# Optimization experiments

Hardware: AMD Instinct MI355X
Metric: run time of the kernel (lower is better)

The kernel has to match this reference:

```python
import jax, jax.numpy as jnp
import numpy as np
import math

B, S, D, H = 4, 2048, 2048, 16
HD = D // H  # 128


def _alibi_slopes(n_heads):
    # standard ALiBi slopes: 2^(-8/n * (h+1))
    return jnp.asarray([2.0 ** (-8.0 / n_heads * (h + 1)) for h in range(n_heads)], dtype=jnp.float32)


def setup_inputs() -> dict:
    key = jax.random.key(0)
    ks = jax.random.split(key, 10)
    w = lambda k: jax.random.normal(k, (D, D), dtype=jnp.float32) * 0.02
    b = lambda k: jax.random.normal(k, (D,), dtype=jnp.float32) * 0.01
    return {
        "hidden_states": jax.random.normal(ks[0], (B, S, D), dtype=jnp.float32),
        "Wq": w(ks[1]), "bq": b(ks[2]),
        "Wk": w(ks[3]), "bk": b(ks[4]),
        "Wv": w(ks[5]), "bv": b(ks[6]),
        "Wo": w(ks[7]), "bo": b(ks[8]),
        "alibi_slopes": _alibi_slopes(H),
    }


def reference(hidden_states, Wq, bq, Wk, bk, Wv, bv, Wo, bo, alibi_slopes):
    Bn, t, _ = hidden_states.shape
    split = lambda x: x.reshape(Bn, t, H, HD).transpose(0, 2, 1, 3)  # [B,H,S,hd]
    q = split(hidden_states @ Wq.T + bq)
    k = split(hidden_states @ Wk.T + bk)
    v = split(hidden_states @ Wv.T + bv)

    scores = jnp.einsum("bhsd,bhtd->bhst", q, k)  # [B,H,S,S]
    pos = jnp.arange(t)
    # alibi bias added BEFORE the 1/sqrt(hd) scaling, as in the torch code
    rel = (pos[None, :] - pos[:, None]).astype(scores.dtype)  # j - i
    bias = alibi_slopes[:, None, None] * rel  # [H,S,S]
    scores = (scores + bias[None]) / math.sqrt(HD)
    # grok-style tanh rescaling
    scores = 30.0 * jnp.tanh(scores / 30.0)
    causal = pos[:, None] >= pos[None, :]  # [S,S]
    scores = jnp.where(causal[None, None], scores, -jnp.inf)
    probs = jax.nn.softmax(scores, axis=-1)
    ctx = jnp.einsum("bhst,bhtd->bhsd", probs, v)
    ctx = ctx.transpose(0, 2, 1, 3).reshape(Bn, t, D)
    return ctx @ Wo.T + bo
```

## Files before the change

### kernel.cpp

```cpp
#include <hip/hip_runtime.h>

typedef unsigned int u32;
typedef unsigned short u16;
typedef __bf16 bf16x8 __attribute__((ext_vector_type(8)));
typedef float f32x4 __attribute__((ext_vector_type(4)));


__device__ __forceinline__ u16 f2bf(float f) {
  u32 u = __builtin_bit_cast(u32, f);
  u32 r = u + 0x7fffu + ((u >> 16) & 1u);
  return (u16)(r >> 16);
}

__device__ __forceinline__ void gload_lds16(const void* g, void* l) {
  __builtin_amdgcn_global_load_lds(
      (__attribute__((address_space(1))) void*)(g),
      (__attribute__((address_space(3))) void*)(l), 16, 0, 0);
}


__global__ __launch_bounds__(256) void convert_kernel(
    const float* __restrict__ hs, const float* __restrict__ wq,
    const float* __restrict__ wk, const float* __restrict__ wv,
    const float* __restrict__ wo,
    u16* __restrict__ hsb, u16* __restrict__ wqb, u16* __restrict__ wkb,
    u16* __restrict__ wvb, u16* __restrict__ wob) {
  long t = (long)blockIdx.x * 256 + threadIdx.x;
  const float* src;
  u16* dst;
  long off;
  if (t < 2097152) {
    src = hs; dst = hsb; off = t << 3;
  } else {
    long u = t - 2097152;
    int wi = (int)(u >> 19);
    off = (u & 524287) << 3;
    if (wi == 0)      { src = wq; dst = wqb; }
    else if (wi == 1) { src = wk; dst = wkb; }
    else if (wi == 2) { src = wv; dst = wvb; }
    else              { src = wo; dst = wob; }
  }
  float4 a = *(const float4*)(src + off);
  float4 b = *(const float4*)(src + off + 4);
  uint4 o;
  o.x = (u32)f2bf(a.x) | ((u32)f2bf(a.y) << 16);
  o.y = (u32)f2bf(a.z) | ((u32)f2bf(a.w) << 16);
  o.z = (u32)f2bf(b.x) | ((u32)f2bf(b.y) << 16);
  o.w = (u32)f2bf(b.z) | ((u32)f2bf(b.w) << 16);
  *(uint4*)(dst + off) = o;
}


template <int OF32>
__global__ __launch_bounds__(512, 2) void gemm256_kernel(
    const u16* __restrict__ A, const u16* __restrict__ Bw,
    const float* __restrict__ bias0, const float* __restrict__ bias1,
    const float* __restrict__ bias2, void* __restrict__ o0,
    void* __restrict__ o1, void* __restrict__ o2, int m_tiles, int n_tiles) {
  __shared__ __align__(16) char L[2][2][2][16384];

  const int tid = threadIdx.x;
  const int lane = tid & 63, w = tid >> 6;
  const int lr = lane & 15, lk = lane >> 4;
  const int wm = (w >> 2) * 128, wn = (w & 3) * 64;

  const int bid = blockIdx.x;
  const int xcd = bid & 7, loc = bid >> 3;
  const int npx = n_tiles >> 3;
  const int n_idx = xcd * npx + loc % npx;
  const int m_idx = loc / npx;
  const int m0 = m_idx * 256, n0 = n_idx * 256;

  const char* Ab = (const char*)A;
  const char* Bb = (const char*)Bw;
  const char* gA[2];
  const char* gB[2];
#pragma unroll
  for (int j = 0; j < 2; j++) {
    const int o = j * 8192 + tid * 16;
    const int row = o >> 6;
    const int c = (o & 63) ^ (((row >> 1) & 3) << 4);
    gA[j] = Ab + (size_t)(m0 + row) * 4096 + c;
    gB[j] = Bb + (size_t)(n0 + row) * 4096 + c;
  }

  auto stage = [&](int t, int kh, int isB) {
    char* Ld = &L[t & 1][isB][kh][0] + tid * 16;
    const int gof = t * 128 + kh * 64;
#pragma unroll
    for (int j = 0; j < 2; j++)
      gload_lds16((isB ? gB[j] : gA[j]) + gof, Ld + j * 8192);
  };
  auto rdA = [&](bf16x8* dst, int buf, int kh, int mset) {
#pragma unroll
    for (int m = 0; m < 4; m++) {
      const int row = wm + mset * 64 + m * 16 + lr;
      const int c = (lk * 16) ^ (((row >> 1) & 3) << 4);
      dst[m] = *(const bf16x8*)(&L[buf][0][kh][0] + row * 64 + c);
    }
  };
  auto rdB = [&](bf16x8* dst, int buf, int kh) {
#pragma unroll
    for (int n = 0; n < 4; n++) {
      const int row = wn + n * 16 + lr;
      const int c = (lk * 16) ^ (((row >> 1) & 3) << 4);
      dst[n] = *(const bf16x8*)(&L[buf][1][kh][0] + row * 64 + c);
    }
  };

  f32x4 acc[2][4][4];
#pragma unroll
  for (int s = 0; s < 2; s++)
#pragma unroll
    for (int m = 0; m < 4; m++)
#pragma unroll
      for (int n = 0; n < 4; n++) acc[s][m][n] = {0.f, 0.f, 0.f, 0.f};

  auto mm = [&](f32x4 (&ac)[4][4], bf16x8* a_, bf16x8* b_) {
    __builtin_amdgcn_s_setprio(1);
#pragma unroll
    for (int m = 0; m < 4; m++)
#pragma unroll
      for (int n = 0; n < 4; n++)
        ac[m][n] = __builtin_amdgcn_mfma_f32_16x16x32_bf16(a_[m], b_[n],
                                                           ac[m][n], 0, 0, 0);
    __builtin_amdgcn_s_setprio(0);
  };

  stage(0, 0, 0); stage(0, 0, 1); stage(0, 1, 0); stage(0, 1, 1);

  bf16x8 aP[4], aQ[4], b0[4], b1[4];
  for (int t = 0; t < 32; ++t) {
    const int buf = t & 1;
    const int t1 = (t + 1 < 32) ? t + 1 : 31;
    asm volatile("s_waitcnt vmcnt(4)" ::: "memory");
    asm volatile("s_barrier" ::: "memory");
    rdA(aP, buf, 0, 0);
    rdB(b0, buf, 0);
    stage(t1, 0, 0);
    if (t) mm(acc[1], aQ, b1);
    rdA(aQ, buf, 0, 1);
    stage(t1, 0, 1);
    mm(acc[0], aP, b0);
    asm volatile("s_waitcnt vmcnt(4)" ::: "memory");
    asm volatile("s_barrier" ::: "memory");
    rdA(aP, buf, 1, 0);
    rdB(b1, buf, 1);
    stage(t1, 1, 0);
    mm(acc[1], aQ, b0);
    rdA(aQ, buf, 1, 1);
    stage(t1, 1, 1);
    mm(acc[0], aP, b1);
  }
  mm(acc[1], aQ, b1);

  const float* bias;
  void* op;
  int nl0;
  if (OF32) {
    bias = bias0; op = o0; nl0 = n0;
  } else {
    const int seg = n0 >> 11;
    bias = seg == 0 ? bias0 : (seg == 1 ? bias1 : bias2);
    op = seg == 0 ? o0 : (seg == 1 ? o1 : o2);
    nl0 = n0 & 2047;
  }
#pragma unroll
  for (int n = 0; n < 4; n++) {
    const int col = nl0 + wn + n * 16 + lr;
    const float bv = bias[col];
#pragma unroll
    for (int s = 0; s < 2; s++)
#pragma unroll
      for (int m = 0; m < 4; m++) {
        const int grow = m0 + wm + s * 64 + m * 16 + lk * 4;
#pragma unroll
        for (int r = 0; r < 4; r++) {
          const float v = acc[s][m][n][r] + bv;
          if (OF32)
            ((float*)op)[(size_t)(grow + r) * 2048 + col] = v;
          else
            ((u16*)op)[(size_t)(grow + r) * 2048 + col] = f2bf(v);
        }
      }
  }
}


__global__ __launch_bounds__(512, 2) void attn_kernel(
    const u16* __restrict__ Qm, const u16* __restrict__ Km,
    const u16* __restrict__ Vm, const float* __restrict__ slopes,
    u16* __restrict__ ctx) {
  __shared__ __align__(16) char Ks[2][64 * 256];
  __shared__ __align__(16) char Vt[128 * 128];
  __shared__ __align__(16) char Pb[8][16 * 128];

  const int bid = blockIdx.x;
  const int sw = (bid & 7) * 64 + (bid >> 3);
  const int bh = sw >> 3, pi = sw & 7;
  const int b = bh >> 4, h = bh & 15;
  const int NTA = 2 * pi + 2;

  const int tid = threadIdx.x;
  const int lane = tid & 63, w = tid >> 6;
  const int lr = lane & 15, lk = lane >> 4;

  const char* Qb = (const char*)Qm + (size_t)b * 2048 * 4096 + h * 256;
  const char* Kb = (const char*)Km + (size_t)b * 2048 * 4096 + h * 256;
  const char* Vb = (const char*)Vm + (size_t)b * 2048 * 4096 + h * 256;

  const float SCALE = 0.08838834764831845f;
  const float sl_c = slopes[h] * SCALE;

  const float C1 = 1.4426950408889634f;
  const float C3 = -5.343315e-4f;
  const float C5 = 2.374806e-7f;
  const float C7 = -1.068005e-10f;

  float zo[16];
#pragma unroll
  for (int nb = 0; nb < 4; nb++)
#pragma unroll
    for (int r = 0; r < 4; r++)
      zo[nb * 4 + r] = sl_c * (float)((lr - lk * 4) + nb * 16 - r);

  const int vd0 = (tid & 15) * 8;
  const int vkv2 = tid >> 4;

  uint4 vr0, vr1;

  auto kvt_of = [&](int it) { return it < NTA ? it : it - NTA; };

  auto stageK = [&](int it, int buf) {
    const int kv0 = kvt_of(it) * 64;
#pragma unroll
    for (int j = 0; j < 2; j++) {
      const int o = j * 8192 + tid * 16;
      const int row = o >> 8, c = (o & 255) ^ ((row & 7) << 4);
      gload_lds16(Kb + (size_t)(kv0 + row) * 4096 + c, Ks[buf] + o);
    }
  };
  auto loadV = [&](int it) {
    const int kv0 = kvt_of(it) * 64;
    vr0 = *(const uint4*)(Vb + (size_t)(kv0 + vkv2 * 2) * 4096 + vd0 * 2);
    vr1 = *(const uint4*)(Vb + (size_t)(kv0 + vkv2 * 2 + 1) * 4096 + vd0 * 2);
  };
  auto writeV = [&]() {
    const u32* p0 = (const u32*)&vr0;
    const u32* p1 = (const u32*)&vr1;
#pragma unroll
    for (int wd = 0; wd < 4; wd++) {
      const u32 ev = __builtin_amdgcn_perm(p1[wd], p0[wd], 0x05040100u);
      const u32 od = __builtin_amdgcn_perm(p1[wd], p0[wd], 0x07060302u);
      const int d0_ = vd0 + 2 * wd, d1_ = d0_ + 1;
      *(u32*)(Vt + d0_ * 128 +
              ((vkv2 * 4) ^ (((d0_ ^ (d0_ >> 3)) & 7) << 4))) = ev;
      *(u32*)(Vt + d1_ * 128 +
              ((vkv2 * 4) ^ (((d1_ ^ (d1_ >> 3)) & 7) << 4))) = od;
    }
  };

  bf16x8 qf[4];
  f32x4 pv[8];
  float rs[4];
  int q0 = 0;

  stageK(0, 0);
  loadV(0);

  for (int it = 0; it < 34; ++it) {
    const int kb = it & 1;
    const int kv0 = kvt_of(it) * 64;

    if (it == 0 || it == NTA) {
      const int st = (it == 0) ? pi : (15 - pi);
      q0 = st * 128 + w * 16;
#pragma unroll
      for (int kc = 0; kc < 4; kc++)
        qf[kc] =
            *(const bf16x8*)(Qb + (size_t)(q0 + lr) * 4096 + kc * 64 + lk * 16);
#pragma unroll
      for (int i = 0; i < 8; i++) pv[i] = {0.f, 0.f, 0.f, 0.f};
      rs[0] = rs[1] = rs[2] = rs[3] = 0.f;
    }

    __syncthreads();
    writeV();
    asm volatile("s_waitcnt vmcnt(0)" ::: "memory");
    __syncthreads();

    if (it + 1 < 34) {
      stageK(it + 1, kb ^ 1);
      loadV(it + 1);
    }

    f32x4 sc[4];
    __builtin_amdgcn_s_setprio(1);
#pragma unroll
    for (int nb = 0; nb < 4; nb++) {
      f32x4 a = {0.f, 0.f, 0.f, 0.f};
      const int krow = nb * 16 + lr;
#pragma unroll
      for (int kc = 0; kc < 4; kc++) {
        const int off = krow * 256 + ((kc * 64 + lk * 16) ^ ((krow & 7) << 4));
        bf16x8 kf = *(const bf16x8*)(Ks[kb] + off);
        a = __builtin_amdgcn_mfma_f32_16x16x32_bf16(qf[kc], kf, a, 0, 0, 0);
      }
      sc[nb] = a;
    }
    __builtin_amdgcn_s_setprio(0);

    const bool diag = (it < NTA) ? (it >= NTA - 2) : (it >= 32);
    const float sb = sl_c * (float)(kv0 - q0);
#pragma unroll
    for (int nb = 0; nb < 4; nb++) {
#pragma unroll
      for (int r = 0; r < 4; r++) {
        float z = fmaf(sc[nb][r], SCALE, zo[nb * 4 + r] + sb);
        z = __builtin_amdgcn_fmed3f(z, -16.0f, 16.0f);
        const float u2 = z * z;
        float hh = fmaf(u2, C7, C5);
        hh = fmaf(u2, hh, C3);
        hh = fmaf(u2, hh, C1);
        float p = exp2f(z * hh);
        if (diag) {
          const int kv = kv0 + nb * 16 + lr;
          const int q = q0 + lk * 4 + r;
          p = (kv <= q) ? p : 0.0f;
        }
        rs[r] += p;
        const int qq = lk * 4 + r;
        const int off = qq * 128 + (((nb * 16 + lr) * 2) ^ ((qq & 7) << 4));
        const u32 ub = __builtin_bit_cast(u32, p);
        *(u16*)(Pb[w] + off) = (u16)((ub + 0x8000u) >> 16);
      }
    }

    __builtin_amdgcn_s_setprio(1);
#pragma unroll
    for (int kc = 0; kc < 2; kc++) {
      const int poff = lr * 128 + ((kc * 64 + lk * 16) ^ ((lr & 7) << 4));
      bf16x8 pf = *(const bf16x8*)(Pb[w] + poff);
#pragma unroll
      for (int db = 0; db < 8; db++) {
        const int d = db * 16 + lr;
        const int voff =
            d * 128 + ((kc * 64 + lk * 16) ^ (((d ^ (d >> 3)) & 7) << 4));
        bf16x8 vf = *(const bf16x8*)(Vt + voff);
        pv[db] = __builtin_amdgcn_mfma_f32_16x16x32_bf16(pf, vf, pv[db], 0, 0, 0);
      }
    }
    __builtin_amdgcn_s_setprio(0);

    if (it == NTA - 1 || it == 33) {
      float inv[4];
#pragma unroll
      for (int r = 0; r < 4; r++) {
        float s = rs[r];
        s += __shfl_xor(s, 1);
        s += __shfl_xor(s, 2);
        s += __shfl_xor(s, 4);
        s += __shfl_xor(s, 8);
        inv[r] = 1.0f / s;
      }
      const size_t baserow = (size_t)b * 2048 + q0 + lk * 4;
#pragma unroll
      for (int db = 0; db < 8; db++)
#pragma unroll
        for (int r = 0; r < 4; r++)
          ctx[(baserow + r) * 2048 + h * 128 + db * 16 + lr] =
              f2bf(pv[db][r] * inv[r]);
    }
  }
}


extern "C" void kernel_launch(void* const* d_in, const int* in_sizes, int n_in,
                              void* d_out, int out_size, void* d_ws,
                              size_t ws_size, hipStream_t stream) {
  const float* hs = (const float*)d_in[0];
  const float* Wq = (const float*)d_in[1];
  const float* bq = (const float*)d_in[2];
  const float* Wk = (const float*)d_in[3];
  const float* bk = (const float*)d_in[4];
  const float* Wv = (const float*)d_in[5];
  const float* bv = (const float*)d_in[6];
  const float* Wo = (const float*)d_in[7];
  const float* bo = (const float*)d_in[8];
  const float* slopes = (const float*)d_in[9];

  char* ws = (char*)d_ws;
  u16* hsb = (u16*)(ws);
  u16* wqb = (u16*)(ws + 33554432);
  u16* wkb = (u16*)(ws + 41943040);
  u16* wvb = (u16*)(ws + 50331648);
  u16* wob = (u16*)(ws + 58720256);
  u16* Qb  = (u16*)(ws + 67108864);
  u16* Kb  = (u16*)(ws + 100663296);
  u16* Vb  = (u16*)(ws + 134217728);
  u16* ctxb = hsb;

  convert_kernel<<<16384, 256, 0, stream>>>(hs, Wq, Wk, Wv, Wo, hsb, wqb, wkb,
                                            wvb, wob);
  gemm256_kernel<0><<<768, 512, 0, stream>>>(hsb, wqb, bq, bk, bv, Qb, Kb, Vb,
                                             32, 24);
  attn_kernel<<<512, 512, 0, stream>>>(Qb, Kb, Vb, slopes, ctxb);
  gemm256_kernel<1><<<256, 512, 0, stream>>>(ctxb, wob, bo, bo, bo, d_out,
                                             d_out, d_out, 32, 8);
}
```

Baseline: 475.7 us.

## Vectorize softmax exp path with packed f32 ops and raise attention occupancy

The per-element score transform (scale, clamp, tanh-polynomial, row sums) is rewritten on two-wide float vectors so the compiler can emit packed FMA/mul instructions. Probability rounding to bf16 now uses the hardware v_cvt_pk_bf16_f32 instruction instead of manual bit arithmetic. The attention kernel's launch bounds go from 2 to 4 blocks per CU, which caps registers per thread to allow more resident waves. The tighter register cap risks spilling, and the bf16 rounding mode changes from round-half-up to the hardware conversion's rounding.

```diff
diff --git a/kernel.cpp b/kernel.cpp
--- a/kernel.cpp
+++ b/kernel.cpp
@@ -4,12 +4,19 @@
 typedef unsigned short u16;
 typedef __bf16 bf16x8 __attribute__((ext_vector_type(8)));
 typedef float f32x4 __attribute__((ext_vector_type(4)));
+typedef float f32x2 __attribute__((ext_vector_type(2)));
 
 
 __device__ __forceinline__ u16 f2bf(float f) {
   u32 u = __builtin_bit_cast(u32, f);
   u32 r = u + 0x7fffu + ((u >> 16) & 1u);
   return (u16)(r >> 16);
+}
+
+__device__ __forceinline__ u32 cvtpk_bf16(float a, float b) {
+  u32 d;
+  asm("v_cvt_pk_bf16_f32 %0, %1, %2" : "=v"(d) : "v"(a), "v"(b));
+  return d;
 }
 
 __device__ __forceinline__ void gload_lds16(const void* g, void* l) {
@@ -187,7 +194,7 @@
 }
 
 
-__global__ __launch_bounds__(512, 2) void attn_kernel(
+__global__ __launch_bounds__(512, 4) void attn_kernel(
     const u16* __restrict__ Qm, const u16* __restrict__ Km,
     const u16* __restrict__ Vm, const float* __restrict__ slopes,
     u16* __restrict__ ctx) {
@@ -212,17 +219,22 @@
   const float SCALE = 0.08838834764831845f;
   const float sl_c = slopes[h] * SCALE;
 
-  const float C1 = 1.4426950408889634f;
-  const float C3 = -5.343315e-4f;
-  const float C5 = 2.374806e-7f;
-  const float C7 = -1.068005e-10f;
-
-  float zo[16];
+  const f32x2 C1v = {1.4426950408889634f, 1.4426950408889634f};
+  const f32x2 C3v = {-5.343315e-4f, -5.343315e-4f};
+  const f32x2 C5v = {2.374806e-7f, 2.374806e-7f};
+  const f32x2 C7v = {-1.068005e-10f, -1.068005e-10f};
+  const f32x2 SC2 = {SCALE, SCALE};
+  const f32x2 NEG16 = {-16.0f, -16.0f};
+  const f32x2 POS16 = {16.0f, 16.0f};
+
+  f32x2 zo2[8];
 #pragma unroll
   for (int nb = 0; nb < 4; nb++)
 #pragma unroll
-    for (int r = 0; r < 4; r++)
-      zo[nb * 4 + r] = sl_c * (float)((lr - lk * 4) + nb * 16 - r);
+    for (int p = 0; p < 2; p++) {
+      zo2[nb * 2 + p][0] = sl_c * (float)((lr - lk * 4) + nb * 16 - (2 * p));
+      zo2[nb * 2 + p][1] = sl_c * (float)((lr - lk * 4) + nb * 16 - (2 * p + 1));
+    }
 
   const int vd0 = (tid & 15) * 8;
   const int vkv2 = tid >> 4;
@@ -262,7 +274,7 @@
 
   bf16x8 qf[4];
   f32x4 pv[8];
-  float rs[4];
+  f32x2 rs2[2];
   int q0 = 0;
 
   stageK(0, 0);
@@ -281,7 +293,8 @@
             *(const bf16x8*)(Qb + (size_t)(q0 + lr) * 4096 + kc * 64 + lk * 16);
 #pragma unroll
       for (int i = 0; i < 8; i++) pv[i] = {0.f, 0.f, 0.f, 0.f};
-      rs[0] = rs[1] = rs[2] = rs[3] = 0.f;
+      rs2[0] = {0.f, 0.f};
+      rs2[1] = {0.f, 0.f};
     }
 
     __syncthreads();
@@ -312,27 +325,37 @@
 
     const bool diag = (it < NTA) ? (it >= NTA - 2) : (it >= 32);
     const float sb = sl_c * (float)(kv0 - q0);
+    const f32x2 sb2 = {sb, sb};
 #pragma unroll
     for (int nb = 0; nb < 4; nb++) {
 #pragma unroll
-      for (int r = 0; r < 4; r++) {
-        float z = fmaf(sc[nb][r], SCALE, zo[nb * 4 + r] + sb);
-        z = __builtin_amdgcn_fmed3f(z, -16.0f, 16.0f);
-        const float u2 = z * z;
-        float hh = fmaf(u2, C7, C5);
-        hh = fmaf(u2, hh, C3);
-        hh = fmaf(u2, hh, C1);
-        float p = exp2f(z * hh);
+      for (int p = 0; p < 2; p++) {
+        f32x2 s2 = {sc[nb][2 * p], sc[nb][2 * p + 1]};
+        f32x2 z = __builtin_elementwise_fma(s2, SC2, zo2[nb * 2 + p] + sb2);
+        z = __builtin_elementwise_max(z, NEG16);
+        z = __builtin_elementwise_min(z, POS16);
+        const f32x2 u2 = z * z;
+        f32x2 hh = __builtin_elementwise_fma(u2, C7v, C5v);
+        hh = __builtin_elementwise_fma(u2, hh, C3v);
+        hh = __builtin_elementwise_fma(u2, hh, C1v);
+        const f32x2 ee = z * hh;
+        float p0 = exp2f(ee[0]);
+        float p1 = exp2f(ee[1]);
         if (diag) {
           const int kv = kv0 + nb * 16 + lr;
-          const int q = q0 + lk * 4 + r;
-          p = (kv <= q) ? p : 0.0f;
+          const int qA = q0 + lk * 4 + 2 * p;
+          p0 = (kv <= qA) ? p0 : 0.0f;
+          p1 = (kv <= qA + 1) ? p1 : 0.0f;
         }
-        rs[r] += p;
-        const int qq = lk * 4 + r;
-        const int off = qq * 128 + (((nb * 16 + lr) * 2) ^ ((qq & 7) << 4));
-        const u32 ub = __builtin_bit_cast(u32, p);
-        *(u16*)(Pb[w] + off) = (u16)((ub + 0x8000u) >> 16);
+        f32x2 pr = {p0, p1};
+        rs2[p] += pr;
+        const u32 pk = cvtpk_bf16(p0, p1);
+        const int qq0 = lk * 4 + 2 * p;
+        const int qq1 = qq0 + 1;
+        const int off0 = qq0 * 128 + (((nb * 16 + lr) * 2) ^ ((qq0 & 7) << 4));
+        const int off1 = qq1 * 128 + (((nb * 16 + lr) * 2) ^ ((qq1 & 7) << 4));
+        *(u16*)(Pb[w] + off0) = (u16)pk;
+        *(u16*)(Pb[w] + off1) = (u16)(pk >> 16);
       }
     }
 
@@ -356,7 +379,7 @@
       float inv[4];
 #pragma unroll
       for (int r = 0; r < 4; r++) {
-        float s = rs[r];
+        float s = (r < 2) ? rs2[0][r & 1] : rs2[1][r & 1];
         s += __shfl_xor(s, 1);
         s += __shfl_xor(s, 2);
         s += __shfl_xor(s, 4);
```

New measurement: 707.3 us. +48.7%, slower.
